# Optimization experiments

Measured on AMD Instinct MI355X. Metric: run time of the kernel, lower is better.

The kernel has to match this reference:

```python
import jax, jax.numpy as jnp
import numpy as np

KEY_DIM = 32
VALUE_DIM = 64
HEADS = 8
CHAN = 256


def conv1x1(x, w, b):
    # x: [b, c, h, w], w: [out, c], b: [out]  (1x1 conv == channel matmul)
    return jnp.einsum('bchw,oc->bohw', x, w) + b[None, :, None, None]


def setup_inputs() -> dict:
    key = jax.random.key(0)
    ks = jax.random.split(key, 9)
    b, c, h, w = 8, CHAN, 128, 128
    qk_dim = KEY_DIM * HEADS   # 256
    v_dim = VALUE_DIM * HEADS  # 512
    s = 0.02
    return {
        'x':  jax.random.normal(ks[0], (b, c, h, w), jnp.float32),
        'Wq': jax.random.normal(ks[1], (qk_dim, c), jnp.float32) * s,
        'bq': jnp.zeros((qk_dim,), jnp.float32),
        'Wk': jax.random.normal(ks[2], (qk_dim, c), jnp.float32) * s,
        'bk': jnp.zeros((qk_dim,), jnp.float32),
        'Wv': jax.random.normal(ks[3], (v_dim, c), jnp.float32) * s,
        'bv': jnp.zeros((v_dim,), jnp.float32),
        'Wo': jax.random.normal(ks[4], (c, v_dim), jnp.float32) * s,
        'bo': jnp.zeros((c,), jnp.float32),
    }


def reference(x, Wq, bq, Wk, bk, Wv, bv, Wo, bo):
    b, c, h, w = x.shape
    n = h * w
    scale = KEY_DIM ** (-0.25)
    # 1x1 conv projections, reshape to [b, heads, d, n]
    q = conv1x1(x, Wq, bq).reshape(b, HEADS, KEY_DIM, n) * scale
    k = conv1x1(x, Wk, bk).reshape(b, HEADS, KEY_DIM, n) * scale
    v = conv1x1(x, Wv, bv).reshape(b, HEADS, VALUE_DIM, n)
    # softmax over sequence positions for keys
    k = jax.nn.softmax(k, axis=-1)
    # norm_queries=True: softmax over key dim for queries
    q = jax.nn.softmax(q, axis=-2)
    # linear attention: context [b,h,d_k,d_v], then output [b,h,d_v,n]
    ctx = jnp.einsum('bhdn,bhen->bhde', k, v)
    out = jnp.einsum('bhdn,bhde->bhen', q, ctx)
    out = out.reshape(b, HEADS * VALUE_DIM, h, w)
    return conv1x1(out, Wo, bo)
```

## Files before the change

kernel.cpp:

```cpp
#include <hip/hip_runtime.h>
#include <hip/hip_bf16.h>
#include <cstddef>


constexpr int   NPIX     = 16384;
constexpr float QK_SCALE = 0.42044820762685725f;
constexpr int   NCH      = 16;

typedef __attribute__((ext_vector_type(8))) short          bf16x8;
typedef __attribute__((ext_vector_type(8))) unsigned short u16x8;
typedef __attribute__((ext_vector_type(4))) float          f32x4;

__device__ __forceinline__ float bf2f(unsigned short v) {
    union { unsigned int u; float f; } c; c.u = ((unsigned int)v) << 16; return c.f;
}
__device__ __forceinline__ unsigned short f2bf(float f) {
    union { __hip_bfloat16 h; unsigned short s; } c; c.h = __float2bfloat16(f); return c.s;
}
__device__ __forceinline__ void gload_lds16(const void* g, void* l) {
    __builtin_amdgcn_global_load_lds(
        (const __attribute__((address_space(1))) unsigned int*)g,
        (__attribute__((address_space(3))) unsigned int*)l, 16, 0, 0);
}

typedef unsigned short lds_row32[32];

__global__ __launch_bounds__(256) void prep(
    const float* __restrict__ Wq, const float* __restrict__ Wk,
    unsigned short* __restrict__ Wqb, unsigned short* __restrict__ Wkb)
{
    const int i = blockIdx.x * 256 + threadIdx.x;
    Wqb[i] = f2bf(Wq[i]);
    Wkb[i] = f2bf(Wk[i]);
}

__global__ __launch_bounds__(256, 2) void kq_proj(
    const float* __restrict__ x,
    const unsigned short* __restrict__ Wkb, const unsigned short* __restrict__ Wqb,
    const float* __restrict__ bk, const float* __restrict__ bq,
    unsigned short* __restrict__ ek, unsigned short* __restrict__ eqT,
    float* __restrict__ ksump2)
{
    __shared__ alignas(16) unsigned char smem[36864];
    lds_row32* As = (lds_row32*)smem;
    unsigned short (*BsT)[40] = (unsigned short(*)[40])(smem + 16384);
    const int b  = blockIdx.z;
    const int m0 = blockIdx.y * 128;
    const int n0 = blockIdx.x * 128;
    const int t  = threadIdx.x;
    const int w  = t >> 6, l = t & 63;
    const int lm = l & 15, lg = l >> 4;
    const int mwl = (w & 1) * 64;
    const int nwl = (w >> 1) * 64;
    const int lgs = (lg ^ ((lm & 3) ^ ((lm >> 2) & 3))) * 8;
    const int r16 = l >> 2;
    const int scb = ((l & 3) ^ ((r16 & 3) ^ ((r16 >> 2) & 3))) * 8;

    const unsigned short* AbK = Wkb + (size_t)m0 * 256;
    const unsigned short* AbQ = Wqb + (size_t)m0 * 256;
    const float* xb = x + (size_t)b * 256 * NPIX + n0;

    const int kr  = t >> 3;
    const int nq4 = (t & 7) * 4;
    const int kslot = kr >> 3, ke = kr & 7;

    f32x4 accK[4][4] = {};
    f32x4 accQ[4][4] = {};
    for (int k0 = 0; k0 < 256; k0 += 32) {
        #pragma unroll
        for (int i = 0; i < 2; ++i) {
            const int row0 = w*32 + i*16;
            gload_lds16(AbK + (size_t)(row0 + r16)*256 + k0 + scb, &As[row0][0]);
            gload_lds16(AbQ + (size_t)(row0 + r16)*256 + k0 + scb, &As[128 + row0][0]);
        }
        {
            const float* src = xb + (size_t)(k0 + kr) * NPIX + nq4;
            f32x4 v[4];
            #pragma unroll
            for (int g = 0; g < 4; ++g)
                v[g] = *(const f32x4*)(src + g * 32);
            #pragma unroll
            for (int g = 0; g < 4; ++g) {
                const int nb   = g*32 + nq4;
                const int slot = (kslot ^ ((nb >> 4) & 3)) * 8 + ke;
                BsT[nb + 0][slot] = f2bf(v[g].x);
                BsT[nb + 1][slot] = f2bf(v[g].y);
                BsT[nb + 2][slot] = f2bf(v[g].z);
                BsT[nb + 3][slot] = f2bf(v[g].w);
            }
        }
        __syncthreads();
        bf16x8 bfr[4];
        #pragma unroll
        for (int j = 0; j < 4; ++j) {
            const int swj = ((nwl >> 4) + j) & 3;
            bfr[j] = *(const bf16x8*)&BsT[nwl + j*16 + lm][(lg ^ swj) * 8];
        }
        #pragma unroll
        for (int i = 0; i < 4; ++i) {
            bf16x8 ak = *(const bf16x8*)&As[mwl + i*16 + lm][lgs];
            bf16x8 aq = *(const bf16x8*)&As[128 + mwl + i*16 + lm][lgs];
            #pragma unroll
            for (int j = 0; j < 4; ++j) {
                accK[i][j] = __builtin_amdgcn_mfma_f32_16x16x32_bf16(ak, bfr[j], accK[i][j], 0, 0, 0);
                accQ[i][j] = __builtin_amdgcn_mfma_f32_16x16x32_bf16(aq, bfr[j], accQ[i][j], 0, 0, 0);
            }
        }
        __syncthreads();
    }

    unsigned short (*Cs)[64][72] = (unsigned short(*)[64][72])smem;
    const int mw = m0 + mwl, nw = n0 + nwl;

    {
        float ksloc[4][4];
        #pragma unroll
        for (int i = 0; i < 4; ++i) {
            const f32x4 bb4 = *(const f32x4*)(bk + mw + i*16 + lg*4);
            #pragma unroll
            for (int r = 0; r < 4; ++r) {
                const int row = i*16 + lg*4 + r;
                float cs = 0.f;
                #pragma unroll
                for (int j = 0; j < 4; ++j) {
                    const int col = j*16 + lm;
                    const unsigned short bs = f2bf(__expf(QK_SCALE * (accK[i][j][r] + bb4[r])));
                    Cs[w][row][col] = bs;
                    cs += bf2f(bs);
                }
                ksloc[i][r] = cs;
            }
        }
        #pragma unroll
        for (int i = 0; i < 4; ++i)
            #pragma unroll
            for (int r = 0; r < 4; ++r) {
                float v = ksloc[i][r];
                v += __shfl_xor(v, 1, 64);
                v += __shfl_xor(v, 2, 64);
                v += __shfl_xor(v, 4, 64);
                v += __shfl_xor(v, 8, 64);
                if (lm == 0) {
                    const int nt2 = blockIdx.x * 2 + (w >> 1);
                    ksump2[((size_t)b*256 + nt2)*256 + mw + i*16 + lg*4 + r] = v;
                }
            }
        __syncthreads();
        unsigned short* dst = ek + ((size_t)b * 256 + mw + l) * NPIX + nw;
        #pragma unroll
        for (int s8 = 0; s8 < 8; ++s8)
            *(u16x8*)(dst + s8*8) = *(const u16x8*)&Cs[w][l][s8*8];
        __syncthreads();
    }

    {
        #pragma unroll
        for (int i = 0; i < 4; ++i) {
            const f32x4 bb4 = *(const f32x4*)(bq + mw + i*16 + lg*4);
            #pragma unroll
            for (int r = 0; r < 4; ++r) {
                const int row = i*16 + lg*4 + r;
                #pragma unroll
                for (int j = 0; j < 4; ++j) {
                    const int col = j*16 + lm;
                    Cs[w][col][row] = f2bf(__expf(QK_SCALE * (accQ[i][j][r] + bb4[r])));
                }
            }
        }
        __syncthreads();
        unsigned short* dst = eqT + ((size_t)b * NPIX + nw + l) * 256 + mw;
        u16x8 vv[8];
        float z0 = 0.f, z1 = 0.f;
        #pragma unroll
        for (int s8 = 0; s8 < 8; ++s8) {
            vv[s8] = *(const u16x8*)&Cs[w][l][s8*8];
            float ps = 0.f;
            #pragma unroll
            for (int u = 0; u < 8; ++u) ps += bf2f(vv[s8][u]);
            if (s8 < 4) z0 += ps; else z1 += ps;
        }
        const float iz0 = 1.0f / z0, iz1 = 1.0f / z1;
        #pragma unroll
        for (int s8 = 0; s8 < 8; ++s8) {
            const float iz = (s8 < 4) ? iz0 : iz1;
            u16x8 o;
            #pragma unroll
            for (int u = 0; u < 8; ++u) o[u] = f2bf(bf2f(vv[s8][u]) * iz);
            *(u16x8*)(dst + s8*8) = o;
        }
    }
}

__global__ __launch_bounds__(256) void ksum_red(
    const float* __restrict__ ksump2, float* __restrict__ ksum)
{
    const int t = threadIdx.x;
    const int row = blockIdx.x * 32 + (t >> 3);
    const int b = row >> 8, c = row & 255;
    const int nt0 = t & 7;
    float s = 0.f;
    #pragma unroll 8
    for (int i = 0; i < 32; ++i)
        s += ksump2[((size_t)b*256 + nt0 + 8*i)*256 + c];
    s += __shfl_xor(s, 1, 64);
    s += __shfl_xor(s, 2, 64);
    s += __shfl_xor(s, 4, 64);
    if (nt0 == 0) ksum[row] = s;
}

__global__ __launch_bounds__(256) void t_mfma(
    const unsigned short* __restrict__ ek, const float* __restrict__ x,
    float* __restrict__ Tpart)
{
    __shared__ alignas(16) unsigned char smem[32768];
    lds_row32* As = (lds_row32*)smem;
    lds_row32* Bs = (lds_row32*)(smem + 16384);
    const int bid  = blockIdx.x;
    const int v    = bid & 7, s = bid >> 3;
    const int gidx = s >> 2, q = s & 3;
    const int group = v + 8 * gidx;
    const int b = group / NCH, chunk = group % NCH;
    const int mt = (q >> 1) * 128, ct = (q & 1) * 128;
    constexpr int CHPX = NPIX / NCH;

    const int t = threadIdx.x;
    const int w = t >> 6, l = t & 63;
    const int lm = l & 15, lg = l >> 4;
    const int mw = (w & 1) * 64, cw = (w >> 1) * 64;
    const int r16 = l >> 2;
    const int scb = ((l & 3) ^ ((r16 & 3) ^ ((r16 >> 2) & 3))) * 8;
    const int lgs = (lg ^ ((lm & 3) ^ ((lm >> 2) & 3))) * 8;
    const int brq = t >> 3;
    const int bc4 = (t & 7) * 4;
    const int bslot = (t & 7) >> 1;
    const int bhalf = (t & 1) * 4;

    const unsigned short* Abase = ek + ((size_t)b*256 + mt) * NPIX;
    const float*          Bbase = x  + ((size_t)b*256 + ct) * NPIX;
    const int p0base = chunk * CHPX;

    f32x4 breg[4];
    f32x4 acc[4][4] = {};

    #pragma unroll
    for (int i = 0; i < 2; ++i) {
        const int row0 = w*32 + i*16;
        gload_lds16(Abase + (size_t)(row0 + r16) * NPIX + p0base + scb, &As[row0][0]);
    }
    #pragma unroll
    for (int it = 0; it < 4; ++it)
        breg[it] = *(const f32x4*)(Bbase + (size_t)(it*32 + brq) * NPIX + p0base + bc4);
    #pragma unroll
    for (int it = 0; it < 4; ++it) {
        const int row = it*32 + brq;
        const int sl = bslot ^ ((row & 3) ^ ((row >> 2) & 3));
        unsigned short o[4] = { f2bf(breg[it].x), f2bf(breg[it].y),
                                f2bf(breg[it].z), f2bf(breg[it].w) };
        *(ushort4*)&Bs[row][sl*8 + bhalf] = *(ushort4*)o;
    }
    __syncthreads();

    constexpr int ITERS = CHPX / 32;
    for (int t8 = 0; t8 < ITERS; ++t8) {
        const int cur = t8 & 1;
        if (t8 < ITERS - 1) {
            const int p0 = p0base + (t8 + 1) * 32;
            #pragma unroll
            for (int i = 0; i < 2; ++i) {
                const int row0 = w*32 + i*16;
                gload_lds16(Abase + (size_t)(row0 + r16) * NPIX + p0 + scb,
                            &As[(cur^1)*128 + row0][0]);
            }
            #pragma unroll
            for (int it = 0; it < 4; ++it)
                breg[it] = *(const f32x4*)(Bbase + (size_t)(it*32 + brq) * NPIX + p0 + bc4);
        }
        bf16x8 afr[4], bfr[4];
        #pragma unroll
        for (int i = 0; i < 4; ++i)
            afr[i] = *(const bf16x8*)&As[cur*128 + mw + i*16 + lm][lgs];
        #pragma unroll
        for (int j = 0; j < 4; ++j)
            bfr[j] = *(const bf16x8*)&Bs[cur*128 + cw + j*16 + lm][lgs];
        #pragma unroll
        for (int i = 0; i < 4; ++i)
            #pragma unroll
            for (int j = 0; j < 4; ++j)
                acc[i][j] = __builtin_amdgcn_mfma_f32_16x16x32_bf16(afr[i], bfr[j], acc[i][j], 0, 0, 0);
        if (t8 < ITERS - 1) {
            #pragma unroll
            for (int it = 0; it < 4; ++it) {
                const int row = it*32 + brq;
                const int sl = bslot ^ ((row & 3) ^ ((row >> 2) & 3));
                unsigned short o[4] = { f2bf(breg[it].x), f2bf(breg[it].y),
                                        f2bf(breg[it].z), f2bf(breg[it].w) };
                *(ushort4*)&Bs[(cur^1)*128 + row][sl*8 + bhalf] = *(ushort4*)o;
            }
        }
        __syncthreads();
    }

    float* dst = Tpart + ((size_t)(b*NCH + chunk) * 256) * 256;
    #pragma unroll
    for (int i = 0; i < 4; ++i)
        #pragma unroll
        for (int r = 0; r < 4; ++r) {
            const int gm = mt + mw + i*16 + lg*4 + r;
            #pragma unroll
            for (int j = 0; j < 4; ++j)
                dst[(size_t)gm * 256 + ct + cw + j*16 + lm] = acc[i][j][r];
        }
}

__global__ __launch_bounds__(256) void treduce(
    float* __restrict__ Tpart, const float* __restrict__ ksum)
{
    const int gid = blockIdx.x * 256 + threadIdx.x;
    const int b   = gid >> 14;
    const int rem = gid & 16383;
    const int r   = rem >> 6;
    const int c4  = (rem & 63) * 4;
    float* base = Tpart + (((size_t)b*NCH) * 256 + r) * 256 + c4;
    f32x4 s = *(f32x4*)base;
    #pragma unroll
    for (int ch = 1; ch < NCH; ++ch) {
        f32x4 v = *(const f32x4*)(base + (size_t)ch * 65536);
        s.x += v.x; s.y += v.y; s.z += v.z; s.w += v.w;
    }
    const float inv = 1.0f / ksum[b*256 + r];
    s.x *= inv; s.y *= inv; s.z *= inv; s.w *= inv;
    *(f32x4*)base = s;
}

__global__ __launch_bounds__(256) void ctx_pass(
    const float* __restrict__ Tpart, const float* __restrict__ Wv,
    const float* __restrict__ bv, float* __restrict__ ctx)
{
    const int gid = blockIdx.x * 256 + threadIdx.x;
    const int b   = gid >> 14;
    const int rem = gid & 16383;
    const int h   = rem >> 11;
    const int de  = rem & 2047;
    const int d   = de >> 6;
    const int e   = de & 63;
    const float* tp = Tpart + (((size_t)b*NCH) * 256 + h*32 + d) * 256;
    const float* wv = Wv + (size_t)(h*64 + e) * 256;
    float sx = 0.f, sy = 0.f, sz = 0.f, sw = 0.f;
    #pragma unroll 8
    for (int c = 0; c < 256; c += 4) {
        f32x4 a = *(const f32x4*)(tp + c);
        f32x4 wv4 = *(const f32x4*)(wv + c);
        sx = fmaf(a.x, wv4.x, sx); sy = fmaf(a.y, wv4.y, sy);
        sz = fmaf(a.z, wv4.z, sz); sw = fmaf(a.w, wv4.w, sw);
    }
    ctx[gid] = (sx + sy) + (sz + sw) + bv[h*64 + e];
}

__global__ __launch_bounds__(256) void mpass(
    const float* __restrict__ ctx, const float* __restrict__ Wo,
    unsigned short* __restrict__ Mb)
{
    const int gid = blockIdx.x * 256 + threadIdx.x;
    const int b   = gid >> 16;
    const int rem = gid & 65535;
    const int o   = rem >> 8;
    const int dg  = rem & 255;
    const int h   = dg >> 5;
    const float* cp = ctx + ((size_t)b*8 + h) * 2048 + (dg & 31) * 64;
    const float* wp = Wo + (size_t)o * 512 + h*64;
    float sx = 0.f, sy = 0.f, sz = 0.f, sw = 0.f;
    #pragma unroll
    for (int e = 0; e < 64; e += 4) {
        f32x4 a = *(const f32x4*)(cp + e);
        f32x4 wv = *(const f32x4*)(wp + e);
        sx = fmaf(a.x, wv.x, sx); sy = fmaf(a.y, wv.y, sy);
        sz = fmaf(a.z, wv.z, sz); sw = fmaf(a.w, wv.w, sw);
    }
    Mb[((size_t)b*256 + o) * 256 + dg] = f2bf((sx + sy) + (sz + sw));
}

__global__ __launch_bounds__(256) void out_mfma(
    const unsigned short* __restrict__ eqT, const unsigned short* __restrict__ Mb,
    const float* __restrict__ bo, float* __restrict__ out)
{
    __shared__ alignas(16) unsigned char smem[32768];
    lds_row32* As0 = (lds_row32*)smem;
    lds_row32* Bs0 = (lds_row32*)(smem + 16384);
    const int b  = blockIdx.z;
    const int m0 = blockIdx.y * 128;
    const int n0 = blockIdx.x * 128;
    const int t  = threadIdx.x;
    const int w  = t >> 6, l = t & 63;
    const int lm = l & 15, lg = l >> 4;
    const int mwl = (w & 1) * 64, nwl = (w >> 1) * 64;
    const int lgs = (lg ^ ((lm & 3) ^ ((lm >> 2) & 3))) * 8;
    const int r16 = l >> 2;
    const int scb = ((l & 3) ^ ((r16 & 3) ^ ((r16 >> 2) & 3))) * 8;

    const unsigned short* Abase = Mb  + ((size_t)b*256 + m0) * 256;
    const unsigned short* Bbase = eqT + ((size_t)b*NPIX + n0) * 256;

    auto stage = [&](int buf, int k0) {
        #pragma unroll
        for (int i = 0; i < 2; ++i) {
            const int row0 = w*32 + i*16;
            gload_lds16(Abase + (size_t)(row0 + r16)*256 + k0 + scb, &As0[buf*128 + row0][0]);
            gload_lds16(Bbase + (size_t)(row0 + r16)*256 + k0 + scb, &Bs0[buf*128 + row0][0]);
        }
    };

    f32x4 acc[4][4] = {};
    stage(0, 0);
    __syncthreads();
    for (int t8 = 0; t8 < 8; ++t8) {
        const int cur = t8 & 1;
        if (t8 < 7) stage(cur ^ 1, (t8 + 1) * 32);
        bf16x8 afr[4], bfr[4];
        #pragma unroll
        for (int i = 0; i < 4; ++i)
            afr[i] = *(const bf16x8*)&As0[cur*128 + mwl + i*16 + lm][lgs];
        #pragma unroll
        for (int j = 0; j < 4; ++j)
            bfr[j] = *(const bf16x8*)&Bs0[cur*128 + nwl + j*16 + lm][lgs];
        #pragma unroll
        for (int i = 0; i < 4; ++i)
            #pragma unroll
            for (int j = 0; j < 4; ++j)
                acc[i][j] = __builtin_amdgcn_mfma_f32_16x16x32_bf16(afr[i], bfr[j], acc[i][j], 0, 0, 0);
        __syncthreads();
    }

    #pragma unroll
    for (int i = 0; i < 4; ++i) {
        const f32x4 bb4 = *(const f32x4*)(bo + m0 + mwl + i*16 + lg*4);
        #pragma unroll
        for (int r = 0; r < 4; ++r) {
            const int gm = m0 + mwl + i*16 + lg*4 + r;
            float* dst = out + ((size_t)b*256 + gm) * NPIX + n0 + nwl;
            #pragma unroll
            for (int j = 0; j < 4; ++j)
                dst[j*16 + lm] = acc[i][j][r] + bb4[r];
        }
    }
}

extern "C" void kernel_launch(void* const* d_in, const int* in_sizes, int n_in,
                              void* d_out, int out_size, void* d_ws, size_t ws_size,
                              hipStream_t stream)
{
    const float* x  = (const float*)d_in[0];
    const float* Wq = (const float*)d_in[1];
    const float* bq = (const float*)d_in[2];
    const float* Wk = (const float*)d_in[3];
    const float* bk = (const float*)d_in[4];
    const float* Wv = (const float*)d_in[5];
    const float* bv = (const float*)d_in[6];
    const float* Wo = (const float*)d_in[7];
    const float* bo = (const float*)d_in[8];
    float* out = (float*)d_out;
    char* wsb = (char*)d_ws;

    if (ws_size < (size_t)169615360) return;

    unsigned short* ek    = (unsigned short*)wsb;
    unsigned short* eqT   = (unsigned short*)(wsb + 67108864);
    float*          Tpart = (float*)(wsb + 134217728);
    float*          ksump2= (float*)(wsb + 134217728);
    float*          ctx   = (float*)(wsb + 167772160);
    float*          ksum  = (float*)(wsb + 168296448);
    unsigned short* Mb    = (unsigned short*)(wsb + 168304640);
    unsigned short* Wqb   = (unsigned short*)(wsb + 169353216);
    unsigned short* Wkb   = (unsigned short*)(wsb + 169484288);

    prep    <<<256,             256, 0, stream>>>(Wq, Wk, Wqb, Wkb);
    kq_proj <<<dim3(128, 2, 8), 256, 0, stream>>>(x, Wkb, Wqb, bk, bq, ek, eqT, ksump2);
    ksum_red<<<64,              256, 0, stream>>>(ksump2, ksum);
    t_mfma  <<<512,             256, 0, stream>>>(ek, x, Tpart);
    treduce <<<512,             256, 0, stream>>>(Tpart, ksum);
    ctx_pass<<<512,             256, 0, stream>>>(Tpart, Wv, bv, ctx);
    mpass   <<<2048,            256, 0, stream>>>(ctx, Wo, Mb);
    out_mfma<<<dim3(128, 2, 8), 256, 0, stream>>>(eqT, Mb, bo, out);
}
```

Baseline: 265.9 us.

## Cache bf16 copy of x in projection kernel and reuse it in T GEMM

After: 271.9 us. 2.2% more time.

```diff
diff --git a/kernel.cpp b/kernel.cpp
--- a/kernel.cpp
+++ b/kernel.cpp
@@ -39,7 +39,7 @@
     const unsigned short* __restrict__ Wkb, const unsigned short* __restrict__ Wqb,
     const float* __restrict__ bk, const float* __restrict__ bq,
     unsigned short* __restrict__ ek, unsigned short* __restrict__ eqT,
-    float* __restrict__ ksump2)
+    unsigned short* __restrict__ xb16, float* __restrict__ ksump2)
 {
     __shared__ alignas(16) unsigned char smem[36864];
     lds_row32* As = (lds_row32*)smem;
@@ -79,14 +79,23 @@
             #pragma unroll
             for (int g = 0; g < 4; ++g)
                 v[g] = *(const f32x4*)(src + g * 32);
+            unsigned short bs16[4][4];
             #pragma unroll
             for (int g = 0; g < 4; ++g) {
+                bs16[g][0] = f2bf(v[g].x); bs16[g][1] = f2bf(v[g].y);
+                bs16[g][2] = f2bf(v[g].z); bs16[g][3] = f2bf(v[g].w);
                 const int nb   = g*32 + nq4;
                 const int slot = (kslot ^ ((nb >> 4) & 3)) * 8 + ke;
-                BsT[nb + 0][slot] = f2bf(v[g].x);
-                BsT[nb + 1][slot] = f2bf(v[g].y);
-                BsT[nb + 2][slot] = f2bf(v[g].z);
-                BsT[nb + 3][slot] = f2bf(v[g].w);
+                BsT[nb + 0][slot] = bs16[g][0];
+                BsT[nb + 1][slot] = bs16[g][1];
+                BsT[nb + 2][slot] = bs16[g][2];
+                BsT[nb + 3][slot] = bs16[g][3];
+            }
+            if (m0 == 0) {
+                unsigned short* xd = xb16 + ((size_t)b*256 + k0 + kr) * NPIX + n0 + nq4;
+                #pragma unroll
+                for (int g = 0; g < 4; ++g)
+                    *(ushort4*)(xd + g*32) = *(ushort4*)bs16[g];
             }
         }
         __syncthreads();
@@ -209,7 +218,7 @@
 }
 
 __global__ __launch_bounds__(256) void t_mfma(
-    const unsigned short* __restrict__ ek, const float* __restrict__ x,
+    const unsigned short* __restrict__ ek, const unsigned short* __restrict__ xb16,
     float* __restrict__ Tpart)
 {
     __shared__ alignas(16) unsigned char smem[32768];
@@ -230,51 +239,27 @@
     const int r16 = l >> 2;
     const int scb = ((l & 3) ^ ((r16 & 3) ^ ((r16 >> 2) & 3))) * 8;
     const int lgs = (lg ^ ((lm & 3) ^ ((lm >> 2) & 3))) * 8;
-    const int brq = t >> 3;
-    const int bc4 = (t & 7) * 4;
-    const int bslot = (t & 7) >> 1;
-    const int bhalf = (t & 1) * 4;
-
-    const unsigned short* Abase = ek + ((size_t)b*256 + mt) * NPIX;
-    const float*          Bbase = x  + ((size_t)b*256 + ct) * NPIX;
+
+    const unsigned short* Abase = ek   + ((size_t)b*256 + mt) * NPIX;
+    const unsigned short* Bbase = xb16 + ((size_t)b*256 + ct) * NPIX;
     const int p0base = chunk * CHPX;
 
-    f32x4 breg[4];
+    auto stage = [&](int buf, int p0) {
+        #pragma unroll
+        for (int i = 0; i < 2; ++i) {
+            const int row0 = w*32 + i*16;
+            gload_lds16(Abase + (size_t)(row0 + r16)*NPIX + p0 + scb, &As[buf*128 + row0][0]);
+            gload_lds16(Bbase + (size_t)(row0 + r16)*NPIX + p0 + scb, &Bs[buf*128 + row0][0]);
+        }
+    };
+
     f32x4 acc[4][4] = {};
-
-    #pragma unroll
-    for (int i = 0; i < 2; ++i) {
-        const int row0 = w*32 + i*16;
-        gload_lds16(Abase + (size_t)(row0 + r16) * NPIX + p0base + scb, &As[row0][0]);
-    }
-    #pragma unroll
-    for (int it = 0; it < 4; ++it)
-        breg[it] = *(const f32x4*)(Bbase + (size_t)(it*32 + brq) * NPIX + p0base + bc4);
-    #pragma unroll
-    for (int it = 0; it < 4; ++it) {
-        const int row = it*32 + brq;
-        const int sl = bslot ^ ((row & 3) ^ ((row >> 2) & 3));
-        unsigned short o[4] = { f2bf(breg[it].x), f2bf(breg[it].y),
-                                f2bf(breg[it].z), f2bf(breg[it].w) };
-        *(ushort4*)&Bs[row][sl*8 + bhalf] = *(ushort4*)o;
-    }
+    stage(0, p0base);
     __syncthreads();
-
     constexpr int ITERS = CHPX / 32;
     for (int t8 = 0; t8 < ITERS; ++t8) {
         const int cur = t8 & 1;
-        if (t8 < ITERS - 1) {
-            const int p0 = p0base + (t8 + 1) * 32;
-            #pragma unroll
-            for (int i = 0; i < 2; ++i) {
-                const int row0 = w*32 + i*16;
-                gload_lds16(Abase + (size_t)(row0 + r16) * NPIX + p0 + scb,
-                            &As[(cur^1)*128 + row0][0]);
-            }
-            #pragma unroll
-            for (int it = 0; it < 4; ++it)
-                breg[it] = *(const f32x4*)(Bbase + (size_t)(it*32 + brq) * NPIX + p0 + bc4);
-        }
+        if (t8 < ITERS - 1) stage(cur ^ 1, p0base + (t8 + 1) * 32);
         bf16x8 afr[4], bfr[4];
         #pragma unroll
         for (int i = 0; i < 4; ++i)
@@ -287,16 +272,6 @@
             #pragma unroll
             for (int j = 0; j < 4; ++j)
                 acc[i][j] = __builtin_amdgcn_mfma_f32_16x16x32_bf16(afr[i], bfr[j], acc[i][j], 0, 0, 0);
-        if (t8 < ITERS - 1) {
-            #pragma unroll
-            for (int it = 0; it < 4; ++it) {
-                const int row = it*32 + brq;
-                const int sl = bslot ^ ((row & 3) ^ ((row >> 2) & 3));
-                unsigned short o[4] = { f2bf(breg[it].x), f2bf(breg[it].y),
-                                        f2bf(breg[it].z), f2bf(breg[it].w) };
-                *(ushort4*)&Bs[(cur^1)*128 + row][sl*8 + bhalf] = *(ushort4*)o;
-            }
-        }
         __syncthreads();
     }
 
@@ -460,22 +435,23 @@
     float* out = (float*)d_out;
     char* wsb = (char*)d_ws;
 
-    if (ws_size < (size_t)169615360) return;
+    if (ws_size < (size_t)236724224) return;
 
     unsigned short* ek    = (unsigned short*)wsb;
     unsigned short* eqT   = (unsigned short*)(wsb + 67108864);
-    float*          Tpart = (float*)(wsb + 134217728);
-    float*          ksump2= (float*)(wsb + 134217728);
-    float*          ctx   = (float*)(wsb + 167772160);
-    float*          ksum  = (float*)(wsb + 168296448);
-    unsigned short* Mb    = (unsigned short*)(wsb + 168304640);
-    unsigned short* Wqb   = (unsigned short*)(wsb + 169353216);
-    unsigned short* Wkb   = (unsigned short*)(wsb + 169484288);
+    unsigned short* xb16  = (unsigned short*)(wsb + 134217728);
+    float*          Tpart = (float*)(wsb + 201326592);
+    float*          ksump2= (float*)(wsb + 201326592);
+    float*          ctx   = (float*)(wsb + 234881024);
+    float*          ksum  = (float*)(wsb + 235405312);
+    unsigned short* Mb    = (unsigned short*)(wsb + 235413504);
+    unsigned short* Wqb   = (unsigned short*)(wsb + 236462080);
+    unsigned short* Wkb   = (unsigned short*)(wsb + 236593152);
 
     prep    <<<256,             256, 0, stream>>>(Wq, Wk, Wqb, Wkb);
-    kq_proj <<<dim3(128, 2, 8), 256, 0, stream>>>(x, Wkb, Wqb, bk, bq, ek, eqT, ksump2);
+    kq_proj <<<dim3(128, 2, 8), 256, 0, stream>>>(x, Wkb, Wqb, bk, bq, ek, eqT, xb16, ksump2);
     ksum_red<<<64,              256, 0, stream>>>(ksump2, ksum);
-    t_mfma  <<<512,             256, 0, stream>>>(ek, x, Tpart);
+    t_mfma  <<<512,             256, 0, stream>>>(ek, xb16, Tpart);
     treduce <<<512,             256, 0, stream>>>(Tpart, ksum);
     ctx_pass<<<512,             256, 0, stream>>>(Tpart, Wv, bv, ctx);
     mpass   <<<2048,            256, 0, stream>>>(ctx, Wo, Mb);
```
